# Kernel optimization log

Hardware: AMD Instinct MI355X
Metric: run time of the kernel (lower is better)

Reference implementation:

```python
import jax, jax.numpy as jnp
import numpy as np

HEADS = 16

def setup_inputs() -> dict:
    key = jax.random.key(0)
    k1, k2, k3 = jax.random.split(key, 3)
    B, E, W = 4, 1024, 2048
    x = jax.random.normal(k1, (B, E, W), dtype=jnp.float32)
    # dense Linear params (bias=True): M ~ randn * ((E+E)/2)^-0.5, b ~ randn / E^2
    M_d = jax.random.normal(k2, (E, E), dtype=jnp.float32) * (E ** -0.5)
    b_d = jax.random.normal(k3, (E,), dtype=jnp.float32) / (E ** 2)
    return {"x": x, "M_d": M_d, "b_d": b_d}


def reference(x, M_d, b_d):
    B, E, W = x.shape
    H = HEADS
    D = E // H
    # NOTE: original code computes self.linear(x) but discards it (KQV = x.view)
    kqv = x.reshape(B, H, D, W)  # [B,H,D,W]
    # scores[b,h,i,j] = sum_d kqv[b,h,d,i]*kqv[b,h,d,j], scaled by E^-0.5
    scores = jnp.einsum('bhdi,bhdj->bhij', kqv, kqv) * (E ** -0.5)
    # causal_factor = tril(ones, diagonal=-1): mask strictly-lower (i>j) to -inf
    i = jnp.arange(W)[:, None]
    j = jnp.arange(W)[None, :]
    scores = jnp.where(i > j, -jnp.inf, scores)
    # softmax over axis -2 (over i, per column j)
    att = jax.nn.softmax(scores, axis=-2)  # [B,H,W,W]
    t = jnp.einsum('bhdi,bhij->bhdj', kqv, att)  # [B,H,D,W]
    t = t.reshape(B, E, W)
    # dense Linear: (B,W,E) @ M + b, transposed back to (B,E,W)
    out = jnp.einsum('bew,ef->bfw', t, M_d) + b_d[None, :, None]
    return out
```

## Files before the change

kernel.cpp:

```cpp
#include <hip/hip_runtime.h>
#include <hip/hip_bf16.h>

constexpr int B  = 4;
constexpr int E  = 1024;
constexpr int Wn = 2048;
constexpr int H  = 16;
constexpr int Dh = 64;

typedef short bf16x8 __attribute__((ext_vector_type(8)));
typedef float f32x4  __attribute__((ext_vector_type(4)));

__device__ inline unsigned short f2bf(float f){
    unsigned int u = __builtin_bit_cast(unsigned int, f);
    u = (u + 0x7fffu + ((u >> 16) & 1u)) >> 16;
    return (unsigned short)u;
}
__device__ inline float bf2f(unsigned short u){
    return __builtin_bit_cast(float, (unsigned int)u << 16);
}
__device__ inline unsigned int pack_bf16_trunc(float lo, float hi){
    return __builtin_amdgcn_perm(__builtin_bit_cast(unsigned int, hi),
                                 __builtin_bit_cast(unsigned int, lo), 0x07060302u);
}
__device__ inline float exp2_fast(float x){ return __builtin_amdgcn_exp2f(x); }

#define GLDS(g, l) __builtin_amdgcn_global_load_lds( \
    (const __attribute__((address_space(1))) void*)(g), \
    (__attribute__((address_space(3))) void*)(l), 16, 0, 0)

__global__ void k_vint(const float* __restrict__ x, unsigned short* __restrict__ xdi){
    int tid = blockIdx.x*256 + threadIdx.x;
    int g   = tid & 255;
    int row = tid >> 8;
    int kgw = g & 3;
    int kv0 = (g >> 2) << 5;
    const float* src = x + (size_t)row*Wn + kv0 + 4*kgw;
    float4 a = *reinterpret_cast<const float4*>(src);
    float4 b = *reinterpret_cast<const float4*>(src + 16);
    union { unsigned short us[8]; uint4 v; } u;
    u.us[0]=f2bf(a.x); u.us[1]=f2bf(a.y); u.us[2]=f2bf(a.z); u.us[3]=f2bf(a.w);
    u.us[4]=f2bf(b.x); u.us[5]=f2bf(b.y); u.us[6]=f2bf(b.z); u.us[7]=f2bf(b.w);
    *reinterpret_cast<uint4*>(xdi + (size_t)row*Wn + kv0 + 8*kgw) = u.v;
}

__global__ void k_xT(const float* __restrict__ x, unsigned short* __restrict__ xT,
                     unsigned short* __restrict__ xQ){
    const float qs = 0.03125f * 1.44269504088896340736f;
    int tid = blockIdx.x*256 + threadIdx.x;
    int w   = tid & (Wn-1);
    int dg  = (tid >> 11) & 7;
    int bh  = tid >> 14;
    const float* src = x + ((size_t)bh*Dh + dg*8)*Wn + w;
    union { unsigned short us[8]; uint4 v; } u, uq;
    #pragma unroll
    for (int i = 0; i < 8; i++){
        float f = src[(size_t)i*Wn];
        u.us[i]  = f2bf(f);
        uq.us[i] = f2bf(f * qs);
    }
    size_t off = ((size_t)bh*Wn + w)*Dh + dg*8;
    *reinterpret_cast<uint4*>(xT + off) = u.v;
    *reinterpret_cast<uint4*>(xQ + off) = uq.v;
}

__global__ void k_MT(const float* __restrict__ M, unsigned short* __restrict__ MT){
    int tid = blockIdx.x*256 + threadIdx.x;
    int f  = tid & (E-1);
    int eg = tid >> 10;
    union { unsigned short us[8]; uint4 v; } u;
    #pragma unroll
    for (int i = 0; i < 8; i++) u.us[i] = f2bf(M[(size_t)(eg*8+i)*E + f]);
    *reinterpret_cast<uint4*>(MT + (size_t)f*E + eg*8) = u.v;
}

__global__ __launch_bounds__(256)
void k_attn(const unsigned short* __restrict__ xT,
            const unsigned short* __restrict__ xQ,
            const unsigned short* __restrict__ xdi,
            unsigned short* __restrict__ tws,
            unsigned short* __restrict__ pacc,
            float* __restrict__ pl){
    __shared__ char Klds[2*8192];
    __shared__ char Vlds[2*8192];

    const int lane = threadIdx.x & 63;
    const int wv   = threadIdx.x >> 6;
    const int jl = lane & 15, kg = lane >> 4;
    const int sw = jl & 7;

    const int p   = blockIdx.x;
    const int xcd = p & 7;
    const int i   = p >> 3;
    const int hh  = i / 24;
    const int j   = i % 24;
    const int bh  = xcd*8 + hh;

    int sb, kvb, kve, half; bool heavy;
    if (j < 8){
        sb = 8 + j; kvb = 0; kve = 1024; heavy = true; half = 0;
    } else {
        int g = 7 - ((j - 8) >> 1);
        if (((j - 8) & 1) == 0){
            sb = 8 + g; kvb = 1024; kve = (sb+1)*128; heavy = true;  half = 1;
        } else {
            sb = g;     kvb = 0;    kve = (sb+1)*128; heavy = false; half = 0;
        }
    }
    const int q0w = sb*128 + wv*32;
    const int nst = (kve - kvb) >> 6;

    const bf16x8* xQr = reinterpret_cast<const bf16x8*>(xQ + (size_t)bh*Wn*Dh);
    bf16x8 bq[2][2];
    #pragma unroll
    for (int jt = 0; jt < 2; jt++){
        bq[jt][0] = xQr[(q0w + jt*16 + jl)*8 + kg];
        bq[jt][1] = xQr[(q0w + jt*16 + jl)*8 + 4 + kg];
    }
    union { bf16x8 v; unsigned short us[8]; } ones;
    #pragma unroll
    for (int i2 = 0; i2 < 8; i2++) ones.us[i2] = 0x3F80;

    f32x4 acc[2][4] = {};
    f32x4 accl[2] = {};

    const char* Kg = (const char*)xT  + (size_t)bh*Wn*128;
    const char* Vg = (const char*)xdi + (size_t)bh*Dh*(Wn*2);
    const int rloc = 8*wv + (lane >> 3);
    const int ksw  = ((lane & 7) ^ (rloc & 7))*16;

    auto STAGE = [&](int buf, int kvT){
        char* Kb = Klds + buf*8192;
        char* Vb = Vlds + buf*8192;
        const char* kg0 = Kg + (size_t)(kvT + rloc)*128 + ksw;
        const char* vg0 = Vg + (size_t)rloc*(Wn*2) + kvT*2 + ksw;
        GLDS(kg0,             Kb + wv*1024);
        GLDS(kg0 + 32*128,    Kb + 4096 + wv*1024);
        GLDS(vg0,             Vb + wv*1024);
        GLDS(vg0 + (size_t)32*(Wn*2), Vb + 4096 + wv*1024);
    };

    auto computeS = [&](int buf, int s, bool dg){
        const char* Kb = Klds + buf*8192;
        const char* Vb = Vlds + buf*8192;
        const int r0 = s*32 + jl, r1 = r0 + 16;
        bf16x8 k0a = *(const bf16x8*)(Kb + r0*128 + ((kg    )^sw)*16);
        bf16x8 k0b = *(const bf16x8*)(Kb + r0*128 + ((kg + 4)^sw)*16);
        bf16x8 k1a = *(const bf16x8*)(Kb + r1*128 + ((kg    )^sw)*16);
        bf16x8 k1b = *(const bf16x8*)(Kb + r1*128 + ((kg + 4)^sw)*16);
        const int vsw = ((s*4 + kg)^sw)*16;
        bf16x8 v0 = *(const bf16x8*)(Vb + (     jl)*128 + vsw);
        bf16x8 v1 = *(const bf16x8*)(Vb + (16 + jl)*128 + vsw);
        bf16x8 v2 = *(const bf16x8*)(Vb + (32 + jl)*128 + vsw);
        bf16x8 v3 = *(const bf16x8*)(Vb + (48 + jl)*128 + vsw);

        #pragma unroll
        for (int jt = 0; jt < 2; jt++){
            f32x4 s0 = {0,0,0,0}, s1 = {0,0,0,0};
            s0 = __builtin_amdgcn_mfma_f32_16x16x32_bf16(k0a, bq[jt][0], s0, 0,0,0);
            s0 = __builtin_amdgcn_mfma_f32_16x16x32_bf16(k0b, bq[jt][1], s0, 0,0,0);
            s1 = __builtin_amdgcn_mfma_f32_16x16x32_bf16(k1a, bq[jt][0], s1, 0,0,0);
            s1 = __builtin_amdgcn_mfma_f32_16x16x32_bf16(k1b, bq[jt][1], s1, 0,0,0);

            union { bf16x8 v; unsigned int w[4]; } bp;
            if (!dg){
                bp.w[0] = pack_bf16_trunc(exp2_fast(s0[0]), exp2_fast(s0[1]));
                bp.w[1] = pack_bf16_trunc(exp2_fast(s0[2]), exp2_fast(s0[3]));
                bp.w[2] = pack_bf16_trunc(exp2_fast(s1[0]), exp2_fast(s1[1]));
                bp.w[3] = pack_bf16_trunc(exp2_fast(s1[2]), exp2_fast(s1[3]));
            } else {
                const int lim = 16*jt + jl;
                float pp[8];
                #pragma unroll
                for (int r = 0; r < 4; r++){
                    int c = 4*kg + r;
                    pp[r]   = (c      <= lim) ? exp2_fast(s0[r]) : 0.f;
                    pp[4+r] = (c + 16 <= lim) ? exp2_fast(s1[r]) : 0.f;
                }
                bp.w[0] = pack_bf16_trunc(pp[0], pp[1]);
                bp.w[1] = pack_bf16_trunc(pp[2], pp[3]);
                bp.w[2] = pack_bf16_trunc(pp[4], pp[5]);
                bp.w[3] = pack_bf16_trunc(pp[6], pp[7]);
            }
            accl[jt] = __builtin_amdgcn_mfma_f32_16x16x32_bf16(ones.v, bp.v, accl[jt], 0,0,0);
            acc[jt][0] = __builtin_amdgcn_mfma_f32_16x16x32_bf16(v0, bp.v, acc[jt][0], 0,0,0);
            acc[jt][1] = __builtin_amdgcn_mfma_f32_16x16x32_bf16(v1, bp.v, acc[jt][1], 0,0,0);
            acc[jt][2] = __builtin_amdgcn_mfma_f32_16x16x32_bf16(v2, bp.v, acc[jt][2], 0,0,0);
            acc[jt][3] = __builtin_amdgcn_mfma_f32_16x16x32_bf16(v3, bp.v, acc[jt][3], 0,0,0);
        }
    };

    STAGE(0, kvb);
    for (int t = 0; t < nst; ++t){
        const int kvT = kvb + 64*t;
        if (t + 1 < nst){
            STAGE((t+1)&1, kvT + 64);
            asm volatile("s_waitcnt vmcnt(4)" ::: "memory");
        } else {
            asm volatile("s_waitcnt vmcnt(0)" ::: "memory");
        }
        __builtin_amdgcn_s_barrier();
        __builtin_amdgcn_sched_barrier(0);
        #pragma unroll
        for (int s = 0; s < 2; ++s){
            const int kv = kvT + 32*s;
            if (kv > q0w) continue;
            computeS(t & 1, s, kv == q0w);
        }
        asm volatile("s_waitcnt lgkmcnt(0)" ::: "memory");
        __builtin_amdgcn_sched_barrier(0);
        __builtin_amdgcn_s_barrier();
    }

    if (!heavy){
        #pragma unroll
        for (int jt = 0; jt < 2; jt++){
            const float inv = 1.0f / accl[jt][0];
            unsigned short* trow = tws + ((size_t)(bh >> 4)*Wn + q0w + jt*16 + jl)*E + (bh & 15)*Dh;
            #pragma unroll
            for (int dt = 0; dt < 4; dt++){
                union { unsigned short us[4]; ushort4 v; } o;
                #pragma unroll
                for (int r = 0; r < 4; r++) o.us[r] = f2bf(acc[jt][dt][r] * inv);
                *reinterpret_cast<ushort4*>(trow + dt*16 + 4*kg) = o.v;
            }
        }
    } else {
        const int qh = sb - 8;
        const size_t slot = (size_t)(bh*8 + qh)*2 + half;
        if (kg == 0){
            pl[slot*128 + wv*32 + jl]      = accl[0][0];
            pl[slot*128 + wv*32 + 16 + jl] = accl[1][0];
        }
        unsigned short* pa = pacc + slot*8192;
        #pragma unroll
        for (int jt = 0; jt < 2; jt++){
            #pragma unroll
            for (int dt = 0; dt < 4; dt++){
                union { unsigned short us[4]; ushort4 v; } o;
                #pragma unroll
                for (int r = 0; r < 4; r++) o.us[r] = f2bf(acc[jt][dt][r]);
                *reinterpret_cast<ushort4*>(pa + (wv*32 + jt*16 + jl)*64 + dt*16 + 4*kg) = o.v;
            }
        }
    }
}

__global__ __launch_bounds__(256) void k_reduce(const unsigned short* __restrict__ pacc,
                                                const float* __restrict__ pl,
                                                unsigned short* __restrict__ tws){
    const int g  = blockIdx.x;
    const int bh = g >> 3, qh = g & 7;
    const int t  = threadIdx.x;
    const int q  = t >> 1;
    const int dbase = (t & 1)*32;
    const size_t slot0 = (size_t)g*2;

    const float inv = 1.0f / (pl[slot0*128 + q] + pl[slot0*128 + 128 + q]);
    const unsigned short* a0 = pacc + slot0*8192 + q*64 + dbase;

    unsigned short* tw = tws + ((size_t)(bh >> 4)*Wn + 1024 + qh*128 + q)*E + (bh & 15)*Dh + dbase;
    #pragma unroll
    for (int i = 0; i < 4; i++){
        union { uint4 v; unsigned short us[8]; } r0, r1, o;
        r0.v = *reinterpret_cast<const uint4*>(a0 + i*8);
        r1.v = *reinterpret_cast<const uint4*>(a0 + 8192 + i*8);
        #pragma unroll
        for (int jj = 0; jj < 8; jj++)
            o.us[jj] = f2bf((bf2f(r0.us[jj]) + bf2f(r1.us[jj])) * inv);
        *reinterpret_cast<uint4*>(tw + i*8) = o.v;
    }
}

__global__ __launch_bounds__(256)
void k_gemm(const unsigned short* __restrict__ MT,
            const unsigned short* __restrict__ tws,
            const float* __restrict__ bd,
            float* __restrict__ out){
    __shared__ char Alds[2*16384];
    __shared__ char Blds[2*16384];

    const int lane = threadIdx.x & 63;
    const int wv   = threadIdx.x >> 6;
    const int jl = lane & 15, kg = lane >> 4;
    const int sw = jl & 7;

    const int p   = blockIdx.x;
    const int blk = (p & 7)*64 + (p >> 3);
    const int b  = blk >> 7;
    const int t2 = blk & 127;
    const int fblk = (t2 >> 4)*128;
    const int wblk = (t2 & 15)*128;
    const int f0 = fblk + (wv >> 1)*64;
    const int w0 = wblk + (wv &  1)*64;

    const char* Ag = (const char*)MT + (size_t)fblk*E*2;
    const char* Bg = (const char*)tws + ((size_t)b*Wn + wblk)*E*2;
    const int rloc = 8*wv + (lane >> 3);
    const int scw  = ((lane & 7) ^ (lane >> 3))*16;

    auto STAGE = [&](int buf, int e0){
        char* Ab = Alds + buf*16384;
        char* Bb = Blds + buf*16384;
        const char* ag = Ag + (size_t)rloc*(E*2) + e0*2 + scw;
        const char* bg = Bg + (size_t)rloc*(E*2) + e0*2 + scw;
        #pragma unroll
        for (int g = 0; g < 4; ++g){
            GLDS(ag + (size_t)g*32*(E*2), Ab + g*4096 + wv*1024);
            GLDS(bg + (size_t)g*32*(E*2), Bb + g*4096 + wv*1024);
        }
    };

    f32x4 acc[4][4] = {};

    auto COMP = [&](int buf){
        const char* Ab = Alds + buf*16384 + ((wv >> 1)*64)*128;
        const char* Bb = Blds + buf*16384 + ((wv &  1)*64)*128;
        #pragma unroll
        for (int h = 0; h < 2; ++h){
            const int cs = ((h*4 + kg) ^ sw)*16;
            bf16x8 am[4], bn[4];
            #pragma unroll
            for (int i = 0; i < 4; i++) am[i] = *(const bf16x8*)(Ab + (i*16 + jl)*128 + cs);
            #pragma unroll
            for (int j = 0; j < 4; j++) bn[j] = *(const bf16x8*)(Bb + (j*16 + jl)*128 + cs);
            #pragma unroll
            for (int i = 0; i < 4; i++)
                #pragma unroll
                for (int j = 0; j < 4; j++)
                    acc[i][j] = __builtin_amdgcn_mfma_f32_16x16x32_bf16(am[i], bn[j], acc[i][j], 0,0,0);
        }
    };

    STAGE(0, 0);
    for (int t = 0; t < 16; ++t){
        if (t < 15){
            STAGE((t+1)&1, (t+1)*64);
            asm volatile("s_waitcnt vmcnt(8)" ::: "memory");
        } else {
            asm volatile("s_waitcnt vmcnt(0)" ::: "memory");
        }
        __builtin_amdgcn_s_barrier();
        __builtin_amdgcn_sched_barrier(0);
        COMP(t & 1);
        asm volatile("s_waitcnt lgkmcnt(0)" ::: "memory");
        __builtin_amdgcn_sched_barrier(0);
        __builtin_amdgcn_s_barrier();
    }

    #pragma unroll
    for (int i = 0; i < 4; i++){
        float bias[4];
        #pragma unroll
        for (int r = 0; r < 4; r++) bias[r] = bd[f0 + i*16 + 4*kg + r];
        #pragma unroll
        for (int j = 0; j < 4; j++){
            #pragma unroll
            for (int r = 0; r < 4; r++){
                out[((size_t)b*E + f0 + i*16 + 4*kg + r)*Wn + w0 + j*16 + jl]
                    = acc[i][j][r] + bias[r];
            }
        }
    }
}

extern "C" void kernel_launch(void* const* d_in, const int* in_sizes, int n_in,
                              void* d_out, int out_size, void* d_ws, size_t ws_size,
                              hipStream_t stream) {
    const float* x  = (const float*)d_in[0];
    const float* Md = (const float*)d_in[1];
    const float* bd = (const float*)d_in[2];
    float* out = (float*)d_out;

    char* ws = (char*)d_ws;
    unsigned short* xT   = (unsigned short*)(ws);
    unsigned short* xQ   = (unsigned short*)(ws + (16u << 20));
    unsigned short* xdi  = (unsigned short*)(ws + (32u << 20));
    unsigned short* MT   = (unsigned short*)(ws + (48u << 20));
    unsigned short* tws  = (unsigned short*)(ws + (50u << 20));
    float*          pl   = (float*)(ws + (66u << 20));
    unsigned short* pacc = (unsigned short*)(ws + (67u << 20));

    hipLaunchKernelGGL(k_vint,   dim3(4096), dim3(256), 0, stream, x, xdi);
    hipLaunchKernelGGL(k_xT,     dim3(4096), dim3(256), 0, stream, x, xT, xQ);
    hipLaunchKernelGGL(k_MT,     dim3(512),  dim3(256), 0, stream, Md, MT);
    hipLaunchKernelGGL(k_attn,   dim3(1536), dim3(256), 0, stream, xT, xQ, xdi, tws, pacc, pl);
    hipLaunchKernelGGL(k_reduce, dim3(512),  dim3(256), 0, stream, pacc, pl, tws);
    hipLaunchKernelGGL(k_gemm,   dim3(B*(E/128)*(Wn/128)), dim3(256), 0, stream, MT, tws, bd, out);
}
```

Baseline: 118.3 us.

## Fuse prep kernels via LDS transpose and split attention into balanced KV chunks

Merges the two fp32-to-bf16 prep kernels into one LDS-tiled transpose kernel. That kernel writes a single scaled K/Q buffer, using sqrt of the combined scale so K and Q share it, plus the V interleave. Attention work is redistributed as 40 fixed-size KV chunks per head, at most 512 keys each, found through constant lookup tables. Every chunk writes partial accumulators, and a generalized reduce sums a variable number of chunks. This targets load imbalance and the redundant reads of x. In exchange, all query blocks now take a partial write and reduce round trip, and more bf16 rounding of partials happens.

```diff
diff --git a/kernel.cpp b/kernel.cpp
--- a/kernel.cpp
+++ b/kernel.cpp
@@ -23,44 +23,71 @@
                                  __builtin_bit_cast(unsigned int, lo), 0x07060302u);
 }
 __device__ inline float exp2_fast(float x){ return __builtin_amdgcn_exp2f(x); }
+__device__ inline int SW(int c){ return c ^ (((c >> 5) & 7) << 2); }
 
 #define GLDS(g, l) __builtin_amdgcn_global_load_lds( \
     (const __attribute__((address_space(1))) void*)(g), \
     (__attribute__((address_space(3))) void*)(l), 16, 0, 0)
 
-__global__ void k_vint(const float* __restrict__ x, unsigned short* __restrict__ xdi){
-    int tid = blockIdx.x*256 + threadIdx.x;
-    int g   = tid & 255;
-    int row = tid >> 8;
-    int kgw = g & 3;
-    int kv0 = (g >> 2) << 5;
-    const float* src = x + (size_t)row*Wn + kv0 + 4*kgw;
-    float4 a = *reinterpret_cast<const float4*>(src);
-    float4 b = *reinterpret_cast<const float4*>(src + 16);
-    union { unsigned short us[8]; uint4 v; } u;
-    u.us[0]=f2bf(a.x); u.us[1]=f2bf(a.y); u.us[2]=f2bf(a.z); u.us[3]=f2bf(a.w);
-    u.us[4]=f2bf(b.x); u.us[5]=f2bf(b.y); u.us[6]=f2bf(b.z); u.us[7]=f2bf(b.w);
-    *reinterpret_cast<uint4*>(xdi + (size_t)row*Wn + kv0 + 8*kgw) = u.v;
-}
-
-__global__ void k_xT(const float* __restrict__ x, unsigned short* __restrict__ xT,
-                     unsigned short* __restrict__ xQ){
-    const float qs = 0.03125f * 1.44269504088896340736f;
-    int tid = blockIdx.x*256 + threadIdx.x;
-    int w   = tid & (Wn-1);
-    int dg  = (tid >> 11) & 7;
-    int bh  = tid >> 14;
-    const float* src = x + ((size_t)bh*Dh + dg*8)*Wn + w;
-    union { unsigned short us[8]; uint4 v; } u, uq;
-    #pragma unroll
-    for (int i = 0; i < 8; i++){
-        float f = src[(size_t)i*Wn];
-        u.us[i]  = f2bf(f);
-        uq.us[i] = f2bf(f * qs);
-    }
-    size_t off = ((size_t)bh*Wn + w)*Dh + dg*8;
-    *reinterpret_cast<uint4*>(xT + off) = u.v;
-    *reinterpret_cast<uint4*>(xQ + off) = uq.v;
+__device__ __constant__ signed char SBT[40] =
+    {3,4,5,6,7,7,8,8,9,9,10,10,11,11,11,12,12,12,13,13,13,14,14,14,15,15,15,15,
+     2,6,10,14, 1,5,9,13, 0,4,8,12};
+__device__ __constant__ signed char CHT[40] =
+    {0,0,0,0,0,1,0,1,0,1,0,1,0,1,2,0,1,2,0,1,2,0,1,2,0,1,2,3,
+     0,1,2,3, 0,1,2,3, 0,1,2,3};
+__device__ __constant__ signed char BASET[16] =
+    {0,1,2,3,4,6,8,10,12,15,18,21,24,28,32,36};
+
+__global__ __launch_bounds__(256) void k_prep(const float* __restrict__ x,
+                                              unsigned short* __restrict__ xS,
+                                              unsigned short* __restrict__ xdi){
+    __shared__ float tile[64*257];
+    const float cs = 0.2123304349f;
+    const int t  = threadIdx.x;
+    const int bh = blockIdx.x >> 3;
+    const int w0 = (blockIdx.x & 7) << 8;
+
+    {
+        const int r = t >> 2, seg = t & 3;
+        const float* src = x + ((size_t)bh*64 + r)*Wn + w0 + seg*64;
+        float* dst = tile + r*257;
+        #pragma unroll
+        for (int i = 0; i < 16; ++i){
+            float4 v = *reinterpret_cast<const float4*>(src + i*4);
+            int c0 = seg*64 + i*4;
+            dst[SW(c0+0)] = v.x; dst[SW(c0+1)] = v.y;
+            dst[SW(c0+2)] = v.z; dst[SW(c0+3)] = v.w;
+        }
+    }
+    __syncthreads();
+
+    {
+        const int kgw = t & 3, g = (t >> 2) & 7, r0 = t >> 5;
+        #pragma unroll
+        for (int rr = 0; rr < 8; ++rr){
+            const int r = r0*8 + rr;
+            const float* base = tile + r*257;
+            const int c0 = g*32 + 4*kgw;
+            union { unsigned short us[8]; uint4 v; } u;
+            #pragma unroll
+            for (int j2 = 0; j2 < 4; ++j2){
+                u.us[j2]   = f2bf(base[SW(c0 + j2)]);
+                u.us[4+j2] = f2bf(base[SW(c0 + 16 + j2)]);
+            }
+            *reinterpret_cast<uint4*>(xdi + ((size_t)bh*64 + r)*Wn + w0 + g*32 + 8*kgw) = u.v;
+        }
+    }
+    {
+        const int w = t;
+        #pragma unroll
+        for (int dg = 0; dg < 8; ++dg){
+            union { unsigned short us[8]; uint4 v; } u;
+            #pragma unroll
+            for (int i = 0; i < 8; ++i)
+                u.us[i] = f2bf(tile[(dg*8 + i)*257 + SW(w)] * cs);
+            *reinterpret_cast<uint4*>(xS + ((size_t)bh*Wn + w0 + w)*64 + dg*8) = u.v;
+        }
+    }
 }
 
 __global__ void k_MT(const float* __restrict__ M, unsigned short* __restrict__ MT){
@@ -74,10 +101,8 @@
 }
 
 __global__ __launch_bounds__(256)
-void k_attn(const unsigned short* __restrict__ xT,
-            const unsigned short* __restrict__ xQ,
+void k_attn(const unsigned short* __restrict__ xS,
             const unsigned short* __restrict__ xdi,
-            unsigned short* __restrict__ tws,
             unsigned short* __restrict__ pacc,
             float* __restrict__ pl){
     __shared__ char Klds[2*8192];
@@ -88,33 +113,27 @@
     const int jl = lane & 15, kg = lane >> 4;
     const int sw = jl & 7;
 
-    const int p   = blockIdx.x;
-    const int xcd = p & 7;
-    const int i   = p >> 3;
-    const int hh  = i / 24;
-    const int j   = i % 24;
-    const int bh  = xcd*8 + hh;
-
-    int sb, kvb, kve, half; bool heavy;
-    if (j < 8){
-        sb = 8 + j; kvb = 0; kve = 1024; heavy = true; half = 0;
-    } else {
-        int g = 7 - ((j - 8) >> 1);
-        if (((j - 8) & 1) == 0){
-            sb = 8 + g; kvb = 1024; kve = (sb+1)*128; heavy = true;  half = 1;
-        } else {
-            sb = g;     kvb = 0;    kve = (sb+1)*128; heavy = false; half = 0;
-        }
-    }
+    const int p    = blockIdx.x;
+    const int xcd  = p & 7;
+    const int q    = p >> 3;
+    const int hh   = q & 7;
+    const int widx = q >> 3;
+    const int bh   = xcd*8 + hh;
+
+    const int sb  = SBT[widx];
+    const int ch  = CHT[widx];
+    const int nst = min(8, (sb+1)*2 - ch*8);
+    const int kvb = ch*512;
+    const bool isLast = (kvb + nst*64 == (sb+1)*128);
+
     const int q0w = sb*128 + wv*32;
-    const int nst = (kve - kvb) >> 6;
-
-    const bf16x8* xQr = reinterpret_cast<const bf16x8*>(xQ + (size_t)bh*Wn*Dh);
+
+    const bf16x8* xSr = reinterpret_cast<const bf16x8*>(xS + (size_t)bh*Wn*Dh);
     bf16x8 bq[2][2];
     #pragma unroll
     for (int jt = 0; jt < 2; jt++){
-        bq[jt][0] = xQr[(q0w + jt*16 + jl)*8 + kg];
-        bq[jt][1] = xQr[(q0w + jt*16 + jl)*8 + 4 + kg];
+        bq[jt][0] = xSr[(q0w + jt*16 + jl)*8 + kg];
+        bq[jt][1] = xSr[(q0w + jt*16 + jl)*8 + 4 + kg];
     }
     union { bf16x8 v; unsigned short us[8]; } ones;
     #pragma unroll
@@ -123,7 +142,7 @@
     f32x4 acc[2][4] = {};
     f32x4 accl[2] = {};
 
-    const char* Kg = (const char*)xT  + (size_t)bh*Wn*128;
+    const char* Kg = (const char*)xS  + (size_t)bh*Wn*128;
     const char* Vg = (const char*)xdi + (size_t)bh*Dh*(Wn*2);
     const int rloc = 8*wv + (lane >> 3);
     const int ksw  = ((lane & 7) ^ (rloc & 7))*16;
@@ -204,43 +223,27 @@
         for (int s = 0; s < 2; ++s){
             const int kv = kvT + 32*s;
             if (kv > q0w) continue;
-            computeS(t & 1, s, kv == q0w);
+            computeS(t & 1, s, isLast && (kv == q0w));
         }
         asm volatile("s_waitcnt lgkmcnt(0)" ::: "memory");
         __builtin_amdgcn_sched_barrier(0);
         __builtin_amdgcn_s_barrier();
     }
 
-    if (!heavy){
-        #pragma unroll
-        for (int jt = 0; jt < 2; jt++){
-            const float inv = 1.0f / accl[jt][0];
-            unsigned short* trow = tws + ((size_t)(bh >> 4)*Wn + q0w + jt*16 + jl)*E + (bh & 15)*Dh;
-            #pragma unroll
-            for (int dt = 0; dt < 4; dt++){
-                union { unsigned short us[4]; ushort4 v; } o;
-                #pragma unroll
-                for (int r = 0; r < 4; r++) o.us[r] = f2bf(acc[jt][dt][r] * inv);
-                *reinterpret_cast<ushort4*>(trow + dt*16 + 4*kg) = o.v;
-            }
-        }
-    } else {
-        const int qh = sb - 8;
-        const size_t slot = (size_t)(bh*8 + qh)*2 + half;
-        if (kg == 0){
-            pl[slot*128 + wv*32 + jl]      = accl[0][0];
-            pl[slot*128 + wv*32 + 16 + jl] = accl[1][0];
-        }
-        unsigned short* pa = pacc + slot*8192;
-        #pragma unroll
-        for (int jt = 0; jt < 2; jt++){
-            #pragma unroll
-            for (int dt = 0; dt < 4; dt++){
-                union { unsigned short us[4]; ushort4 v; } o;
-                #pragma unroll
-                for (int r = 0; r < 4; r++) o.us[r] = f2bf(acc[jt][dt][r]);
-                *reinterpret_cast<ushort4*>(pa + (wv*32 + jt*16 + jl)*64 + dt*16 + 4*kg) = o.v;
-            }
+    const int slot = bh*40 + BASET[sb] + ch;
+    if (kg == 0){
+        pl[(size_t)slot*128 + wv*32 + jl]      = accl[0][0];
+        pl[(size_t)slot*128 + wv*32 + 16 + jl] = accl[1][0];
+    }
+    unsigned short* pa = pacc + (size_t)slot*8192;
+    #pragma unroll
+    for (int jt = 0; jt < 2; jt++){
+        #pragma unroll
+        for (int dt = 0; dt < 4; dt++){
+            union { unsigned short us[4]; ushort4 v; } o;
+            #pragma unroll
+            for (int r = 0; r < 4; r++) o.us[r] = f2bf(acc[jt][dt][r]);
+            *reinterpret_cast<ushort4*>(pa + (wv*32 + jt*16 + jl)*64 + dt*16 + 4*kg) = o.v;
         }
     }
 }
@@ -249,24 +252,35 @@
                                                 const float* __restrict__ pl,
                                                 unsigned short* __restrict__ tws){
     const int g  = blockIdx.x;
-    const int bh = g >> 3, qh = g & 7;
+    const int bh = g >> 4, sb = g & 15;
     const int t  = threadIdx.x;
-    const int q  = t >> 1;
-    const int dbase = (t & 1)*32;
-    const size_t slot0 = (size_t)g*2;
-
-    const float inv = 1.0f / (pl[slot0*128 + q] + pl[slot0*128 + 128 + q]);
-    const unsigned short* a0 = pacc + slot0*8192 + q*64 + dbase;
-
-    unsigned short* tw = tws + ((size_t)(bh >> 4)*Wn + 1024 + qh*128 + q)*E + (bh & 15)*Dh + dbase;
-    #pragma unroll
-    for (int i = 0; i < 4; i++){
-        union { uint4 v; unsigned short us[8]; } r0, r1, o;
-        r0.v = *reinterpret_cast<const uint4*>(a0 + i*8);
-        r1.v = *reinterpret_cast<const uint4*>(a0 + 8192 + i*8);
-        #pragma unroll
-        for (int jj = 0; jj < 8; jj++)
-            o.us[jj] = f2bf((bf2f(r0.us[jj]) + bf2f(r1.us[jj])) * inv);
+    const int qq = t >> 1;
+    const int db = (t & 1)*32;
+    const int nch   = (sb + 4) >> 2;
+    const int slot0 = bh*40 + BASET[sb];
+
+    float l = 0.f;
+    float a[32];
+    #pragma unroll
+    for (int i = 0; i < 32; ++i) a[i] = 0.f;
+    for (int c = 0; c < nch; ++c){
+        l += pl[(size_t)(slot0 + c)*128 + qq];
+        const unsigned short* pa = pacc + (size_t)(slot0 + c)*8192 + qq*64 + db;
+        #pragma unroll
+        for (int i = 0; i < 4; ++i){
+            union { uint4 v; unsigned short us[8]; } r0;
+            r0.v = *reinterpret_cast<const uint4*>(pa + i*8);
+            #pragma unroll
+            for (int j2 = 0; j2 < 8; ++j2) a[i*8 + j2] += bf2f(r0.us[j2]);
+        }
+    }
+    const float inv = 1.0f / l;
+    unsigned short* tw = tws + ((size_t)(bh >> 4)*Wn + sb*128 + qq)*E + (bh & 15)*Dh + db;
+    #pragma unroll
+    for (int i = 0; i < 4; ++i){
+        union { uint4 v; unsigned short us[8]; } o;
+        #pragma unroll
+        for (int j2 = 0; j2 < 8; ++j2) o.us[j2] = f2bf(a[i*8 + j2] * inv);
         *reinterpret_cast<uint4*>(tw + i*8) = o.v;
     }
 }
@@ -372,18 +386,16 @@
     float* out = (float*)d_out;
 
     char* ws = (char*)d_ws;
-    unsigned short* xT   = (unsigned short*)(ws);
-    unsigned short* xQ   = (unsigned short*)(ws + (16u << 20));
-    unsigned short* xdi  = (unsigned short*)(ws + (32u << 20));
-    unsigned short* MT   = (unsigned short*)(ws + (48u << 20));
-    unsigned short* tws  = (unsigned short*)(ws + (50u << 20));
-    float*          pl   = (float*)(ws + (66u << 20));
-    unsigned short* pacc = (unsigned short*)(ws + (67u << 20));
-
-    hipLaunchKernelGGL(k_vint,   dim3(4096), dim3(256), 0, stream, x, xdi);
-    hipLaunchKernelGGL(k_xT,     dim3(4096), dim3(256), 0, stream, x, xT, xQ);
+    unsigned short* xS   = (unsigned short*)(ws);
+    unsigned short* xdi  = (unsigned short*)(ws + (16u << 20));
+    unsigned short* MT   = (unsigned short*)(ws + (32u << 20));
+    unsigned short* tws  = (unsigned short*)(ws + (34u << 20));
+    float*          pl   = (float*)(ws + (50u << 20));
+    unsigned short* pacc = (unsigned short*)(ws + (52u << 20));
+
+    hipLaunchKernelGGL(k_prep,   dim3(512),  dim3(256), 0, stream, x, xS, xdi);
     hipLaunchKernelGGL(k_MT,     dim3(512),  dim3(256), 0, stream, Md, MT);
-    hipLaunchKernelGGL(k_attn,   dim3(1536), dim3(256), 0, stream, xT, xQ, xdi, tws, pacc, pl);
-    hipLaunchKernelGGL(k_reduce, dim3(512),  dim3(256), 0, stream, pacc, pl, tws);
+    hipLaunchKernelGGL(k_attn,   dim3(2560), dim3(256), 0, stream, xS, xdi, pacc, pl);
+    hipLaunchKernelGGL(k_reduce, dim3(1024), dim3(256), 0, stream, pacc, pl, tws);
     hipLaunchKernelGGL(k_gemm,   dim3(B*(E/128)*(Wn/128)), dim3(256), 0, stream, MT, tws, bd, out);
 }
```

Measured after the change: 113.8 us. 3.7% less time.
